# Optimization experiments

Hardware: AMD Instinct MI355X
Metric: run time of the kernel (lower is better)

## Reference

```python
import jax, jax.numpy as jnp
import numpy as np
from jax import lax

P_SIZE, STRIDE, KSIZE = 128, 64, 31
EPS = 1e-6

def _pupil_basis(K):
    # masked polynomial (Zernike-like) basis over the unit pupil, unit-RMS normalized
    c = np.linspace(-1.0, 1.0, K)
    xx, yy = np.meshgrid(c, c, indexing='xy')
    r2 = xx ** 2 + yy ** 2
    mask = (r2 <= 1.0).astype(np.float32)
    polys = []
    for deg in range(1, 5):  # all monomials x^i y^j, 1 <= i+j <= 4  -> 14 terms
        for i in range(deg + 1):
            polys.append((xx ** (deg - i)) * (yy ** i))
    basis = np.stack(polys).astype(np.float32) * mask  # [14,K,K]
    rms = np.sqrt((basis ** 2).sum((1, 2)) / mask.sum()) + 1e-8
    return jnp.asarray(basis / rms[:, None, None]), jnp.asarray(mask)

BASIS, MASK = _pupil_basis(KSIZE)
# per-RGB wavelength scaling of the aberration phase (green = reference)
WL_SCALE = jnp.asarray((0.53 / np.array([0.61, 0.53, 0.47], np.float32)))


def _zernike_psfs(coeffs):
    # coeffs [N, 14] -> PSF kernels [N, 3, K, K], each normalized to sum 1
    phase = jnp.einsum('nz,zij->nij', coeffs, BASIS)            # [N,K,K]
    phase = phase[:, None] * WL_SCALE[None, :, None, None]       # [N,3,K,K]
    field = MASK * jnp.exp(1j * (2.0 * jnp.pi) * phase)          # complex64
    spec = jnp.fft.fft2(jnp.fft.ifftshift(field, axes=(-2, -1)))
    psf = jnp.abs(jnp.fft.fftshift(spec, axes=(-2, -1))) ** 2
    return psf / (psf.sum((-2, -1), keepdims=True) + EPS)


def _mlp(coords, w1, b1, w2, b2, w3, b3):
    h = jnp.tanh(coords @ w1 + b1)
    h = jnp.tanh(h @ w2 + b2)
    return h @ w3 + b3


def setup_inputs() -> dict:
    key = jax.random.key(0)
    ks = jax.random.split(key, 4)
    B, C, H, W = 4, 3, 768, 768
    hid, nz = 64, 14
    return {
        'x_hat': jax.random.uniform(ks[0], (B, C, H, W), jnp.float32),
        'w1': jax.random.normal(ks[1], (2, hid), jnp.float32) * float(1.0 / np.sqrt(2.0)),
        'b1': jnp.zeros((hid,), jnp.float32),
        'w2': jax.random.normal(ks[2], (hid, hid), jnp.float32) * float(1.0 / np.sqrt(hid)),
        'b2': jnp.zeros((hid,), jnp.float32),
        'w3': jax.random.normal(ks[3], (hid, nz), jnp.float32) * 0.05,
        'b3': jnp.zeros((nz,), jnp.float32),
        'gamma': jnp.asarray(2.2, jnp.float32),
    }


def reference(x_hat, w1, b1, w2, b2, w3, b3, gamma):
    B, C, H, W = x_hat.shape
    P, S, K = P_SIZE, STRIDE, KSIZE
    # gamma de-correction to linear intensity
    x_lin = (jax.nn.relu(x_hat) + EPS) ** gamma
    pad_h = (-(H - P)) % S
    pad_w = (-(W - P)) % S
    x_pad = jnp.pad(x_lin, ((0, 0), (0, 0), (0, pad_h), (0, pad_w)), mode='reflect') if (pad_h or pad_w) else x_lin
    Hp, Wp = x_pad.shape[2], x_pad.shape[3]
    n_h = (Hp - P) // S + 1
    n_w = (Wp - P) // S + 1
    N = n_h * n_w
    # ----- unfold: gather overlapping P x P patches -----
    ih = np.arange(n_h)[:, None] * S + np.arange(P)[None, :]   # [n_h,P]
    iw = np.arange(n_w)[:, None] * S + np.arange(P)[None, :]   # [n_w,P]
    patches = x_pad[:, :, ih[:, None, :, None], iw[None, :, None, :]]  # [B,C,n_h,n_w,P,P]
    patches = patches.transpose(0, 2, 3, 1, 4, 5).reshape(B * N, C, P, P)
    # ----- patch-center normalized coords in [-1,1] -----
    yc = (np.arange(n_h) * S + P / 2) / Hp * 2 - 1
    xc = (np.arange(n_w) * S + P / 2) / Wp * 2 - 1
    gy, gx = np.meshgrid(yc, xc, indexing='ij')
    coords = jnp.asarray(np.stack([gy.ravel(), gx.ravel()], 1).astype(np.float32))  # [N,2]
    coords = jnp.tile(coords, (B, 1))                                                # [B*N,2]
    # ----- spatially-varying PSF per patch -----
    coeffs = _mlp(coords, w1, b1, w2, b2, w3, b3)   # [B*N,14]
    kernels = _zernike_psfs(coeffs)                  # [B*N,3,K,K]
    kernels = kernels[..., ::-1, ::-1]               # flip -> true convolution
    # ----- per-patch grouped convolution (C == C_k path) -----
    BN = B * N
    pad = K // 2
    pp = jnp.pad(patches, ((0, 0), (0, 0), (pad, pad), (pad, pad)))
    lhs = pp.reshape(1, BN * C, P + 2 * pad, P + 2 * pad)
    rhs = kernels.reshape(BN * C, 1, K, K)
    y = lax.conv_general_dilated(lhs, rhs, (1, 1), 'VALID',
                                 dimension_numbers=('NCHW', 'OIHW', 'NCHW'),
                                 feature_group_count=BN * C)
    y = y.reshape(BN, C, P, P)
    # ----- Hann window + overlap-add reconstruction -----
    hann = 0.5 * (1.0 - jnp.cos(2.0 * jnp.pi * jnp.arange(P, dtype=x_hat.dtype) / P))
    window = hann[:, None] * hann[None, :]
    y = y * window
    y = y.reshape(B, n_h, n_w, C, P, P).transpose(0, 3, 1, 2, 4, 5)  # [B,C,n_h,n_w,P,P]
    out = jnp.zeros((B, C, Hp, Wp), x_hat.dtype)
    out = out.at[:, :, ih[:, None, :, None], iw[None, :, None, :]].add(y)
    norm = jnp.zeros((Hp, Wp), x_hat.dtype)
    norm = norm.at[ih[:, None, :, None], iw[None, :, None, :]].add(jnp.broadcast_to(window, (n_h, n_w, P, P)))
    out = out / (norm + EPS)
    out = out[:, :, :H, :W]
    # gamma re-correction back to display space
    return (jnp.clip(out, 0.0) + EPS) ** (1.0 / gamma)
```

## Files before the change

### kernel.cpp

```cpp
#include <hip/hip_runtime.h>
#include <math.h>

#define EPSF 1e-6f
#define NB   4
#define NC   3
#define HH   768
#define KS   31
#define KK   961
#define NHW  11
#define NN   121
#define NZ   14
#define HID  64

#define XLIN_OFF  0
#define XLIN_F    3538944
#define BASIS_OFF (XLIN_OFF + XLIN_F)
#define MASK_OFF  (BASIS_OFF + 13456)
#define COEF_OFF  (MASK_OFF + 964)
#define KERN_OFF  (COEF_OFF + 1696)
#define WNC_U4    (31 * 96)

typedef _Float16 h8 __attribute__((ext_vector_type(8)));
typedef float f32x16 __attribute__((ext_vector_type(16)));

__device__ __forceinline__ unsigned pack_h2(float a, float b) {
    return __builtin_bit_cast(unsigned, __builtin_amdgcn_cvt_pkrtz(a, b));
}

__device__ __forceinline__ float hann_f(int p) {
    return 0.5f * (1.0f - cosf(6.283185307179586f * (float)p / 128.0f));
}

__device__ __forceinline__ void gll16(const uint4* g, uint4* l) {
    __builtin_amdgcn_global_load_lds(
        (const __attribute__((address_space(1))) unsigned*)g,
        (__attribute__((address_space(3))) unsigned*)l,
        16, 0, 0);
}

__global__ void k_front(const float4* __restrict__ x, const float* __restrict__ gp,
                        uint2* __restrict__ y, int n4,
                        const float* __restrict__ w1, const float* __restrict__ b1,
                        const float* __restrict__ w2, const float* __restrict__ b2,
                        const float* __restrict__ w3, const float* __restrict__ b3,
                        float* __restrict__ ws) {
    __shared__ float h1[HID], h2v[HID];
    __shared__ float red[256];
    __shared__ float srms[NZ];
    __shared__ float scnt;
    int bid = blockIdx.x, t = threadIdx.x;
    if (bid < NN) {
        int n = bid;
        int a = n / NHW, bw = n - a * NHW;
        float gy = (float)((((double)(a * 64)  + 64.0) / 768.0) * 2.0 - 1.0);
        float gx = (float)((((double)(bw * 64) + 64.0) / 768.0) * 2.0 - 1.0);
        if (t < HID) h1[t] = tanhf(gy * w1[t] + gx * w1[HID + t] + b1[t]);
        __syncthreads();
        if (t < HID) {
            float acc2 = b2[t];
            for (int k = 0; k < HID; ++k) acc2 += h1[k] * w2[k * HID + t];
            h2v[t] = tanhf(acc2);
        }
        __syncthreads();
        if (t < NZ) {
            float acc3 = b3[t];
            for (int k = 0; k < HID; ++k) acc3 += h2v[k] * w3[k * NZ + t];
            ws[COEF_OFF + n * NZ + t] = acc3;
        }
        return;
    }
    if (bid == NN) {
        float* basis = ws + BASIS_OFF;
        float* mask  = ws + MASK_OFF;
        int tid = t;
        double lsq[NZ];
        #pragma unroll
        for (int z = 0; z < NZ; ++z) lsq[z] = 0.0;
        double lcnt = 0.0;
        for (int pix = tid; pix < KK; pix += 256) {
            int i = pix / 31, j = pix - i * 31;
            double xx = (j == 30) ? 1.0 : (-1.0 + (double)j * (2.0 / 30.0));
            double yy = (i == 30) ? 1.0 : (-1.0 + (double)i * (2.0 / 30.0));
            double r2 = xx * xx + yy * yy;
            float m = (r2 <= 1.0) ? 1.0f : 0.0f;
            mask[pix] = m;
            lcnt += (double)m;
            #pragma unroll
            for (int deg = 1; deg <= 4; ++deg) {
                #pragma unroll
                for (int ii = 0; ii <= deg; ++ii) {
                    const int z = deg * (deg + 1) / 2 - 1 + ii;
                    double px = 1.0, py = 1.0;
                    #pragma unroll
                    for (int q = 0; q < deg - ii; ++q) px *= xx;
                    #pragma unroll
                    for (int q = 0; q < ii; ++q) py *= yy;
                    float bf = (float)(px * py) * m;
                    basis[z * KK + pix] = bf;
                    lsq[z] += (double)bf * (double)bf;
                }
            }
        }
        for (int q = 0; q < NZ + 1; ++q) {
            red[tid] = (q < NZ) ? (float)lsq[q] : (float)lcnt;
            __syncthreads();
            for (int s = 128; s > 0; s >>= 1) {
                if (tid < s) red[tid] += red[tid + s];
                __syncthreads();
            }
            if (tid == 0) { if (q < NZ) srms[q] = red[0]; else scnt = red[0]; }
            __syncthreads();
        }
        if (tid < NZ) srms[tid] = sqrtf(srms[tid] / scnt) + 1e-8f;
        __syncthreads();
        for (int pix = tid; pix < KK; pix += 256) {
            #pragma unroll
            for (int z = 0; z < NZ; ++z)
                basis[z * KK + pix] = basis[z * KK + pix] / srms[z];
        }
        return;
    }
    float g = *gp;
    int i0 = (bid - (NN + 1)) * blockDim.x + t;
    int gs = (gridDim.x - (NN + 1)) * blockDim.x;
    for (int i = i0; i < n4; i += gs) {
        float4 v = x[i];
        uint2 o;
        o.x = pack_h2(__powf(fmaxf(v.x, 0.0f) + EPSF, g), __powf(fmaxf(v.y, 0.0f) + EPSF, g));
        o.y = pack_h2(__powf(fmaxf(v.z, 0.0f) + EPSF, g), __powf(fmaxf(v.w, 0.0f) + EPSF, g));
        y[i] = o;
    }
}

__global__ void k_psf(float* __restrict__ ws) {
    __shared__ float fre[KK], fim[KK], gre[KK], gim[KK], sS[KK];
    __shared__ float twc[KS], tws[KS], cf[NZ], red[128];
    __shared__ float pc[31 * 104];
    int blk = blockIdx.x;
    int n = blk / 3, c = blk - n * 3;
    int tid = threadIdx.x;
    const float* basis = ws + BASIS_OFF;
    const float* mask  = ws + MASK_OFF;
    if (tid < NZ) cf[tid] = ws[COEF_OFF + n * NZ + tid];
    if (tid < KS) {
        float ang = -6.283185307179586f * (float)tid / 31.0f;
        float s, co;
        sincosf(ang, &s, &co);
        twc[tid] = co; tws[tid] = s;
    }
    const float wl = (c == 0) ? (0.53f / 0.61f) : ((c == 1) ? 1.0f : (0.53f / 0.47f));
    __syncthreads();
    for (int pix = tid; pix < KK; pix += 128) {
        float ph = 0.0f;
        #pragma unroll
        for (int z = 0; z < NZ; ++z) ph += cf[z] * basis[z * KK + pix];
        float ang = 6.283185307179586f * (wl * ph);
        float s, co;
        sincosf(ang, &s, &co);
        float m = mask[pix];
        fre[pix] = m * co;
        fim[pix] = m * s;
    }
    __syncthreads();
    for (int pix = tid; pix < KK; pix += 128) {
        int i = pix / 31, q = pix - i * 31;
        float ar = 0.0f, ai = 0.0f;
        int m = 0;
        const float* br = &fre[i * 31];
        const float* bi = &fim[i * 31];
        #pragma unroll
        for (int j = 0; j < 31; ++j) {
            float tc = twc[m], ts = tws[m];
            float xr = br[j], xi = bi[j];
            ar += xr * tc - xi * ts;
            ai += xr * ts + xi * tc;
            m += q; if (m >= 31) m -= 31;
        }
        gre[pix] = ar; gim[pix] = ai;
    }
    __syncthreads();
    float lsum = 0.0f;
    for (int pix = tid; pix < KK; pix += 128) {
        int p = pix / 31, q = pix - p * 31;
        float ar = 0.0f, ai = 0.0f;
        int m = 0;
        #pragma unroll
        for (int i2 = 0; i2 < 31; ++i2) {
            float tc = twc[m], ts = tws[m];
            float xr = gre[i2 * 31 + q], xi = gim[i2 * 31 + q];
            ar += xr * tc - xi * ts;
            ai += xr * ts + xi * tc;
            m += p; if (m >= 31) m -= 31;
        }
        float sv = ar * ar + ai * ai;
        sS[pix] = sv;
        lsum += sv;
    }
    red[tid] = lsum;
    __syncthreads();
    for (int s = 64; s > 0; s >>= 1) {
        if (tid < s) red[tid] += red[tid + s];
        __syncthreads();
    }
    float tot = red[0] + EPSF;
    for (int idx = tid; idx < 31 * 104; idx += 128) {
        int v = idx / 104, x = idx - v * 104;
        int iv = 15 - v; if (iv < 0) iv += 31;
        float val = 0.0f;
        int t = x - 31;
        if ((unsigned)t < 31u) {
            int iu = 15 - t; if (iu < 0) iu += 31;
            val = sS[iu * 31 + iv] / tot;
        }
        pc[idx] = val;
    }
    __syncthreads();
    uint4* wp = (uint4*)(ws + KERN_OFF) + (size_t)(n * 3 + c) * WNC_U4;
    for (int idx = tid; idx < 31 * 96; idx += 128) {
        int v = idx / 96, s = idx - v * 96;
        const float* p = &pc[v * 104 + s];
        uint4 u;
        u.x = pack_h2(p[0], p[1]);
        u.y = pack_h2(p[2], p[3]);
        u.z = pack_h2(p[4], p[5]);
        u.w = pack_h2(p[6], p[7]);
        wp[idx] = u;
    }
}

__global__ __launch_bounds__(256, 5) void k_conv(const float* __restrict__ ws,
                                                 const float* __restrict__ gp,
                                                 float* __restrict__ out) {
    __shared__ unsigned short sT[94 * 104];
    __shared__ uint4 At[2][4][88];
    __shared__ float hT[128];
    int bid = blockIdx.x;
    int swz = (bid & 7) * 216 + (bid >> 3);
    int bc = swz % 12;
    int tile = swz / 12;
    int c = bc % 3;
    int tx = tile % 12, ta = tile / 12;
    int y0 = ta * 64, x0 = tx * 64;
    int tid = threadIdx.x;
    const unsigned short* xlc = (const unsigned short*)ws + (size_t)bc * (HH * HH);
    if (tid < 128) hT[tid] = hann_f(tid);
    for (int idx = tid; idx < 94 * 96; idx += 256) {
        int q = idx / 94, col = idx - (idx / 94) * 94;
        int pi = y0 + q - 15, pj = x0 + col - 15;
        unsigned short hv = 0;
        if (q < 94 && (unsigned)pi < 768u && (unsigned)pj < 768u)
            hv = xlc[pi * HH + pj];
        sT[col * 104 + q] = hv;
    }
    int lane = tid & 63, wave = tid >> 6;
    int qy = wave >> 1, qx = wave & 1;
    int nI = lane & 31, k8 = lane >> 5;
    int cx = qx * 32 + nI;
    bool vy0 = (ta <= 10), vy1 = (ta >= 1);
    bool vx0 = (tx <= 10), vx1 = (tx >= 1);
    const uint4* wtab = (const uint4*)(ws + KERN_OFF);
    int aaw = ta - (wave >> 1), bbw = tx - (wave & 1);
    bool vw = ((unsigned)aaw < 11u) && ((unsigned)bbw < 11u);
    int nnw = vw ? (aaw * NHW + bbw) : 0;
    const uint4* stab = wtab + (size_t)(nnw * 3 + c) * WNC_U4;
    gll16(stab + lane, &At[0][wave][0]);
    if (lane < 24) gll16(stab + 64 + lane, &At[0][wave][64]);
    __syncthreads();

    int tA0 = 8 * k8 - nI + 31;
    f32x16 acc[4];
    #pragma unroll
    for (int p = 0; p < 4; ++p) acc[p] = (f32x16)(0.0f);
    int buf = 0;
    #pragma unroll 1
    for (int v = 0; v < 31; ++v) {
        if (v < 30) {
            const uint4* src = stab + (v + 1) * 96;
            gll16(src + lane, &At[buf ^ 1][wave][0]);
            if (lane < 24) gll16(src + 64 + lane, &At[buf ^ 1][wave][64]);
        }
        h8 B[4];
        const uint4* cb = (const uint4*)&sT[(cx + v) * 104 + qy * 32 + k8 * 8];
        #pragma unroll
        for (int o = 0; o < 4; ++o)
            B[o] = __builtin_bit_cast(h8, cb[o * 2]);
        #pragma unroll
        for (int p = 0; p < 4; ++p) {
            #pragma unroll
            for (int o = 0; o < 4; ++o) {
                uint4 u = At[buf][p][tA0 + o * 16];
                h8 A = __builtin_bit_cast(h8, u);
                acc[p] = __builtin_amdgcn_mfma_f32_32x32x16_f16(
                    A, B[o], acc[p], 0, 0, 0);
            }
        }
        __syncthreads();
        buf ^= 1;
    }
    float ig = 1.0f / (*gp);
    float hx = hT[cx];
    float wxc0 = vx0 ? hx : 0.0f;
    float wxc1 = vx1 ? (1.0f - hx) : 0.0f;
    float sw = wxc0 + wxc1;
    float* ob = out + (size_t)bc * (HH * HH) + (size_t)y0 * HH + x0;
    #pragma unroll
    for (int reg = 0; reg < 16; ++reg) {
        int rr = (reg & 3) + 8 * (reg >> 2) + 4 * k8;
        int ry = qy * 32 + rr;
        float hy = hT[ry];
        float wy0 = vy0 ? hy : 0.0f;
        float wy1 = vy1 ? (1.0f - hy) : 0.0f;
        float val = wy0 * (wxc0 * acc[0][reg] + wxc1 * acc[1][reg])
                  + wy1 * (wxc0 * acc[2][reg] + wxc1 * acc[3][reg]);
        float vv = val / ((wy0 + wy1) * sw + EPSF);
        ob[(size_t)ry * HH + cx] = __powf(fmaxf(vv, 0.0f) + EPSF, ig);
    }
}

extern "C" void kernel_launch(void* const* d_in, const int* in_sizes, int n_in,
                              void* d_out, int out_size, void* d_ws, size_t ws_size,
                              hipStream_t stream) {
    const float* x  = (const float*)d_in[0];
    const float* w1 = (const float*)d_in[1];
    const float* b1 = (const float*)d_in[2];
    const float* w2 = (const float*)d_in[3];
    const float* b2 = (const float*)d_in[4];
    const float* w3 = (const float*)d_in[5];
    const float* b3 = (const float*)d_in[6];
    const float* gp = (const float*)d_in[7];
    float* out = (float*)d_out;
    float* ws  = (float*)d_ws;

    int ntot = NB * NC * HH * HH;
    k_front<<<2048, 256, 0, stream>>>((const float4*)x, gp, (uint2*)(ws + XLIN_OFF),
                                      ntot / 4, w1, b1, w2, b2, w3, b3, ws);
    k_psf<<<NN * NC, 128, 0, stream>>>(ws);
    k_conv<<<NB * NC * 144, 256, 0, stream>>>(ws, gp, out);
}
```

Before: 281.6 us.

## Enlarge conv tiles to 128x64 output rows per block to share kernel loads

Each conv block now computes a 128-row by 64-column output region instead of 64x64, with each wave owning a 32-row stripe and both 32-column halves. The staged input tile in shared memory grows accordingly. Kernel weights for the row-overlapping patch are shared across the vertical pair, so six kernel slices are streamed per block instead of eight per two blocks. This halves the grid and doubles accumulators per wave, which lowers occupancy (launch bounds drop to 2) and raises register and LDS pressure.

```diff
diff --git a/kernel.cpp b/kernel.cpp
--- a/kernel.cpp
+++ b/kernel.cpp
@@ -228,92 +228,127 @@
     }
 }
 
-__global__ __launch_bounds__(256, 5) void k_conv(const float* __restrict__ ws,
+__global__ __launch_bounds__(256, 2) void k_conv(const float* __restrict__ ws,
                                                  const float* __restrict__ gp,
                                                  float* __restrict__ out) {
-    __shared__ unsigned short sT[94 * 104];
-    __shared__ uint4 At[2][4][88];
+    __shared__ unsigned short sT[94 * 168];
+    __shared__ uint4 At[2][6][88];
     __shared__ float hT[128];
     int bid = blockIdx.x;
-    int swz = (bid & 7) * 216 + (bid >> 3);
+    int swz = (bid & 7) * 108 + (bid >> 3);
     int bc = swz % 12;
     int tile = swz / 12;
     int c = bc % 3;
-    int tx = tile % 12, ta = tile / 12;
-    int y0 = ta * 64, x0 = tx * 64;
+    int tx = tile % 12, tv = tile / 12;
+    int y0 = tv * 128, x0 = tx * 64;
     int tid = threadIdx.x;
     const unsigned short* xlc = (const unsigned short*)ws + (size_t)bc * (HH * HH);
     if (tid < 128) hT[tid] = hann_f(tid);
-    for (int idx = tid; idx < 94 * 96; idx += 256) {
-        int q = idx / 94, col = idx - (idx / 94) * 94;
+    for (int idx = tid; idx < 94 * 160; idx += 256) {
+        int q = idx / 94, col = idx - q * 94;
         int pi = y0 + q - 15, pj = x0 + col - 15;
         unsigned short hv = 0;
-        if (q < 94 && (unsigned)pi < 768u && (unsigned)pj < 768u)
+        if (q < 158 && (unsigned)pi < 768u && (unsigned)pj < 768u)
             hv = xlc[pi * HH + pj];
-        sT[col * 104 + q] = hv;
+        sT[col * 168 + q] = hv;
     }
     int lane = tid & 63, wave = tid >> 6;
-    int qy = wave >> 1, qx = wave & 1;
     int nI = lane & 31, k8 = lane >> 5;
-    int cx = qx * 32 + nI;
-    bool vy0 = (ta <= 10), vy1 = (ta >= 1);
+    int a0 = 2 * tv;
     bool vx0 = (tx <= 10), vx1 = (tx >= 1);
+    bool lowW = (wave < 2);
+    bool vBv = lowW ? (a0 >= 1) : (a0 + 1 <= 10);
     const uint4* wtab = (const uint4*)(ws + KERN_OFF);
-    int aaw = ta - (wave >> 1), bbw = tx - (wave & 1);
-    bool vw = ((unsigned)aaw < 11u) && ((unsigned)bbw < 11u);
-    int nnw = vw ? (aaw * NHW + bbw) : 0;
-    const uint4* stab = wtab + (size_t)(nnw * 3 + c) * WNC_U4;
-    gll16(stab + lane, &At[0][wave][0]);
-    if (lane < 24) gll16(stab + 64 + lane, &At[0][wave][64]);
+    int sva = a0 - 1 + (wave >> 1);
+    int shb = tx - (wave & 1);
+    bool sval = ((unsigned)sva < 11u) && ((unsigned)shb < 11u);
+    int snn = sval ? (sva * NHW + shb) : 0;
+    const uint4* stab1 = wtab + (size_t)(snn * 3 + c) * WNC_U4;
+    int shb2 = tx - wave;
+    bool sval2 = lowW && (a0 + 1 <= 10) && ((unsigned)shb2 < 11u);
+    int snn2 = sval2 ? ((a0 + 1) * NHW + shb2) : 0;
+    const uint4* stab2 = wtab + (size_t)(snn2 * 3 + c) * WNC_U4;
+    gll16(stab1 + lane, &At[0][wave][0]);
+    if (lane < 24) gll16(stab1 + 64 + lane, &At[0][wave][64]);
+    if (lowW) {
+        gll16(stab2 + lane, &At[0][4 + wave][0]);
+        if (lane < 24) gll16(stab2 + 64 + lane, &At[0][4 + wave][64]);
+    }
     __syncthreads();
 
     int tA0 = 8 * k8 - nI + 31;
-    f32x16 acc[4];
-    #pragma unroll
-    for (int p = 0; p < 4; ++p) acc[p] = (f32x16)(0.0f);
+    int tB = lowW ? 0 : 4;
+    const unsigned short* bB0 = &sT[nI * 168 + wave * 32 + k8 * 8];
+    const unsigned short* bB1 = &sT[(32 + nI) * 168 + wave * 32 + k8 * 8];
+    f32x16 cAA0 = (f32x16)(0.0f), cAB0 = (f32x16)(0.0f);
+    f32x16 cBA0 = (f32x16)(0.0f), cBB0 = (f32x16)(0.0f);
+    f32x16 cAA1 = (f32x16)(0.0f), cAB1 = (f32x16)(0.0f);
+    f32x16 cBA1 = (f32x16)(0.0f), cBB1 = (f32x16)(0.0f);
     int buf = 0;
     #pragma unroll 1
     for (int v = 0; v < 31; ++v) {
         if (v < 30) {
-            const uint4* src = stab + (v + 1) * 96;
-            gll16(src + lane, &At[buf ^ 1][wave][0]);
-            if (lane < 24) gll16(src + 64 + lane, &At[buf ^ 1][wave][64]);
-        }
-        h8 B[4];
-        const uint4* cb = (const uint4*)&sT[(cx + v) * 104 + qy * 32 + k8 * 8];
-        #pragma unroll
-        for (int o = 0; o < 4; ++o)
-            B[o] = __builtin_bit_cast(h8, cb[o * 2]);
-        #pragma unroll
-        for (int p = 0; p < 4; ++p) {
-            #pragma unroll
-            for (int o = 0; o < 4; ++o) {
-                uint4 u = At[buf][p][tA0 + o * 16];
-                h8 A = __builtin_bit_cast(h8, u);
-                acc[p] = __builtin_amdgcn_mfma_f32_32x32x16_f16(
-                    A, B[o], acc[p], 0, 0, 0);
+            const uint4* s1 = stab1 + (v + 1) * 96;
+            gll16(s1 + lane, &At[buf ^ 1][wave][0]);
+            if (lane < 24) gll16(s1 + 64 + lane, &At[buf ^ 1][wave][64]);
+            if (lowW) {
+                const uint4* s2 = stab2 + (v + 1) * 96;
+                gll16(s2 + lane, &At[buf ^ 1][4 + wave][0]);
+                if (lane < 24) gll16(s2 + 64 + lane, &At[buf ^ 1][4 + wave][64]);
             }
         }
+        h8 B0[4], B1[4];
+        #pragma unroll
+        for (int o = 0; o < 4; ++o) {
+            B0[o] = __builtin_bit_cast(h8, *(const uint4*)(bB0 + v * 168 + o * 16));
+            B1[o] = __builtin_bit_cast(h8, *(const uint4*)(bB1 + v * 168 + o * 16));
+        }
+        const uint4* aA0 = &At[buf][2][0] + tA0;
+        const uint4* aA1 = &At[buf][3][0] + tA0;
+        const uint4* aB0 = &At[buf][tB][0] + tA0;
+        const uint4* aB1 = &At[buf][tB + 1][0] + tA0;
+        #pragma unroll
+        for (int o = 0; o < 4; ++o) {
+            h8 fA0 = __builtin_bit_cast(h8, aA0[o * 16]);
+            h8 fA1 = __builtin_bit_cast(h8, aA1[o * 16]);
+            h8 fB0 = __builtin_bit_cast(h8, aB0[o * 16]);
+            h8 fB1 = __builtin_bit_cast(h8, aB1[o * 16]);
+            cAA0 = __builtin_amdgcn_mfma_f32_32x32x16_f16(fA0, B0[o], cAA0, 0, 0, 0);
+            cAB0 = __builtin_amdgcn_mfma_f32_32x32x16_f16(fA1, B0[o], cAB0, 0, 0, 0);
+            cBA0 = __builtin_amdgcn_mfma_f32_32x32x16_f16(fB0, B0[o], cBA0, 0, 0, 0);
+            cBB0 = __builtin_amdgcn_mfma_f32_32x32x16_f16(fB1, B0[o], cBB0, 0, 0, 0);
+            cAA1 = __builtin_amdgcn_mfma_f32_32x32x16_f16(fA0, B1[o], cAA1, 0, 0, 0);
+            cAB1 = __builtin_amdgcn_mfma_f32_32x32x16_f16(fA1, B1[o], cAB1, 0, 0, 0);
+            cBA1 = __builtin_amdgcn_mfma_f32_32x32x16_f16(fB0, B1[o], cBA1, 0, 0, 0);
+            cBB1 = __builtin_amdgcn_mfma_f32_32x32x16_f16(fB1, B1[o], cBB1, 0, 0, 0);
+        }
         __syncthreads();
         buf ^= 1;
     }
     float ig = 1.0f / (*gp);
-    float hx = hT[cx];
-    float wxc0 = vx0 ? hx : 0.0f;
-    float wxc1 = vx1 ? (1.0f - hx) : 0.0f;
-    float sw = wxc0 + wxc1;
+    float hx0 = hT[nI];
+    float hx1 = hT[32 + nI];
+    float wx00 = vx0 ? hx0 : 0.0f;
+    float wx01 = vx1 ? (1.0f - hx0) : 0.0f;
+    float wx10 = vx0 ? hx1 : 0.0f;
+    float wx11 = vx1 ? (1.0f - hx1) : 0.0f;
+    float sw0 = wx00 + wx01, sw1 = wx10 + wx11;
     float* ob = out + (size_t)bc * (HH * HH) + (size_t)y0 * HH + x0;
     #pragma unroll
     for (int reg = 0; reg < 16; ++reg) {
-        int rr = (reg & 3) + 8 * (reg >> 2) + 4 * k8;
-        int ry = qy * 32 + rr;
-        float hy = hT[ry];
-        float wy0 = vy0 ? hy : 0.0f;
-        float wy1 = vy1 ? (1.0f - hy) : 0.0f;
-        float val = wy0 * (wxc0 * acc[0][reg] + wxc1 * acc[1][reg])
-                  + wy1 * (wxc0 * acc[2][reg] + wxc1 * acc[3][reg]);
-        float vv = val / ((wy0 + wy1) * sw + EPSF);
-        ob[(size_t)ry * HH + cx] = __powf(fmaxf(vv, 0.0f) + EPSF, ig);
+        int r = (reg & 3) + 8 * (reg >> 2) + 4 * k8;
+        int rr = wave * 32 + r;
+        float wA = hT[rr];
+        float wB = vBv ? (1.0f - wA) : 0.0f;
+        float wyn = wA + wB;
+        float v0 = wA * (wx00 * cAA0[reg] + wx01 * cAB0[reg])
+                 + wB * (wx00 * cBA0[reg] + wx01 * cBB0[reg]);
+        float v1 = wA * (wx10 * cAA1[reg] + wx11 * cAB1[reg])
+                 + wB * (wx10 * cBA1[reg] + wx11 * cBB1[reg]);
+        float o0 = v0 / (wyn * sw0 + EPSF);
+        float o1 = v1 / (wyn * sw1 + EPSF);
+        ob[(size_t)rr * HH + nI]      = __powf(fmaxf(o0, 0.0f) + EPSF, ig);
+        ob[(size_t)rr * HH + 32 + nI] = __powf(fmaxf(o1, 0.0f) + EPSF, ig);
     }
 }
 
@@ -335,5 +370,5 @@
     k_front<<<2048, 256, 0, stream>>>((const float4*)x, gp, (uint2*)(ws + XLIN_OFF),
                                       ntot / 4, w1, b1, w2, b2, w3, b3, ws);
     k_psf<<<NN * NC, 128, 0, stream>>>(ws);
-    k_conv<<<NB * NC * 144, 256, 0, stream>>>(ws, gp, out);
-}
+    k_conv<<<NB * NC * 72, 256, 0, stream>>>(ws, gp, out);
+}
```

New measurement: 310.9 us. 1.1x slower.
